# Kernel optimization log

Measured on AMD Instinct MI355X. Metric: run time of the kernel, lower is better.

The kernel has to match this reference:

```python
import jax, jax.numpy as jnp
import numpy as np

B, HW, ENC = 64, 14, 2048
L, V, E, D, A = 20, 10000, 512, 512, 512
T = L - 1  # max decode length (one caption forced to length L)


def setup_inputs() -> dict:
    key = jax.random.key(0)
    ks = jax.random.split(key, 16)

    def p(k, shape, s=0.02):
        return jax.random.normal(k, shape, jnp.float32) * s

    cl = jax.random.randint(ks[2], (B,), 5, L + 1).at[0].set(L)
    return {
        "encoder_out": jax.random.normal(ks[0], (B, HW, HW, ENC), jnp.float32),
        "encoded_captions": jax.random.randint(ks[1], (B, L), 0, V),
        "caption_lengths": cl[:, None].astype(jnp.int32),
        "emb": jax.random.uniform(ks[3], (V, E), jnp.float32, -0.1, 0.1),
        "W_ih": p(ks[4], (4 * D, E + ENC)), "b_ih": jnp.zeros((4 * D,), jnp.float32),
        "W_hh": p(ks[5], (4 * D, D)), "b_hh": jnp.zeros((4 * D,), jnp.float32),
        "W_init_h": p(ks[6], (D, ENC)), "b_init_h": jnp.zeros((D,), jnp.float32),
        "W_init_c": p(ks[7], (D, ENC)), "b_init_c": jnp.zeros((D,), jnp.float32),
        "W_fbeta": p(ks[8], (ENC, D)), "b_fbeta": jnp.zeros((ENC,), jnp.float32),
        "W_fc": jax.random.uniform(ks[9], (V, D), jnp.float32, -0.1, 0.1), "b_fc": jnp.zeros((V,), jnp.float32),
        "W_enc_att": p(ks[10], (A, ENC)), "b_enc_att": jnp.zeros((A,), jnp.float32),
        "W_dec_att": p(ks[11], (A, D)), "b_dec_att": jnp.zeros((A,), jnp.float32),
        "W_full_att": p(ks[12], (1, A)), "b_full_att": jnp.zeros((1,), jnp.float32),
    }


def _decode(encoder_out, encoded_captions, caption_lengths, emb,
            W_ih, b_ih, W_hh, b_hh, W_init_h, b_init_h, W_init_c, b_init_c,
            W_fbeta, b_fbeta, W_fc, b_fc, W_enc_att, b_enc_att,
            W_dec_att, b_dec_att, W_full_att, b_full_att):
    b = encoder_out.shape[0]
    enc = encoder_out.reshape(b, -1, encoder_out.shape[-1])  # [B, P, ENC]
    cl = caption_lengths[:, 0]
    sort_ind = jnp.argsort(-cl)  # descending by caption length
    cl = cl[sort_ind]
    enc = enc[sort_ind]
    caps = encoded_captions[sort_ind]
    decode_lengths = cl - 1  # per-sample number of decode steps

    mean_enc = jnp.mean(enc, axis=1)  # [B, ENC]
    h0 = mean_enc @ W_init_h.T + b_init_h
    c0 = mean_enc @ W_init_c.T + b_init_c

    embeddings = emb[caps]  # [B, L, E]
    # encoder-side attention projection is h-independent: precompute once
    att1 = jnp.einsum('bpe,ae->bpa', enc, W_enc_att) + b_enc_att  # [B, P, A]

    xs_emb = jnp.swapaxes(embeddings[:, :T], 0, 1)  # [T, B, E]
    masks = decode_lengths[None, :] > jnp.arange(T)[:, None]  # [T, B]
    # Note: torch slices h[:batch_size_t]; since batch is length-sorted descending,
    # masking inactive rows (freeze state, zero outputs) computes identical values.

    def step(carry, xs):
        h, c = carry
        emb_t, mask = xs
        # Bahdanau soft attention
        att2 = h @ W_dec_att.T + b_dec_att  # [B, A]
        e = jnp.einsum('bpa,a->bp', jnp.tanh(att1 + att2[:, None, :]), W_full_att[0]) + b_full_att[0]
        alpha = jax.nn.softmax(e, axis=1)  # [B, P]
        awe = jnp.einsum('bp,bpe->be', alpha, enc)  # [B, ENC]
        gate = jax.nn.sigmoid(h @ W_fbeta.T + b_fbeta)
        x = jnp.concatenate([emb_t, gate * awe], axis=1)  # [B, E+ENC]
        # LSTMCell (torch gate order: i, f, g, o)
        gates = x @ W_ih.T + b_ih + h @ W_hh.T + b_hh
        i, f, g, o = jnp.split(gates, 4, axis=1)
        c_new = jax.nn.sigmoid(f) * c + jax.nn.sigmoid(i) * jnp.tanh(g)
        h_new = jax.nn.sigmoid(o) * jnp.tanh(c_new)
        preds = h_new @ W_fc.T + b_fc  # dropout = identity in eval
        m = mask[:, None]
        h = jnp.where(m, h_new, h)
        c = jnp.where(m, c_new, c)
        return (h, c), (jnp.where(m, preds, 0.0), jnp.where(m, alpha, 0.0))

    (_, _), (preds, alphas) = jax.lax.scan(step, (h0, c0), (xs_emb, masks))
    predictions = jnp.swapaxes(preds, 0, 1)  # [B, T, V]
    alphas = jnp.swapaxes(alphas, 0, 1)      # [B, T, P]
    return predictions, caps, alphas, sort_ind


def reference(encoder_out, encoded_captions, caption_lengths, emb,
              W_ih, b_ih, W_hh, b_hh, W_init_h, b_init_h, W_init_c, b_init_c,
              W_fbeta, b_fbeta, W_fc, b_fc, W_enc_att, b_enc_att,
              W_dec_att, b_dec_att, W_full_att, b_full_att):
    return _decode(encoder_out, encoded_captions, caption_lengths, emb,
                   W_ih, b_ih, W_hh, b_hh, W_init_h, b_init_h, W_init_c, b_init_c,
                   W_fbeta, b_fbeta, W_fc, b_fc, W_enc_att, b_enc_att,
                   W_dec_att, b_dec_att, W_full_att, b_full_att)
```

## Files before the change

kernel.cpp:

```cpp
#include <hip/hip_runtime.h>
#include <math.h>

#define Bb 64
#define Pp 196
#define ENCd 2048
#define Lc 20
#define Tt 19
#define Vv 10000
#define Ee 512
#define Dd 512
#define Aa 512
#define K2 2560
#define KG 3072
#define G4 2048

#define OUT_PRED 0ll
#define OUT_CAPS 12160000ll
#define OUT_ALPH 12161280ll
#define OUT_SIND 12399616ll

typedef unsigned short ushort_t;
typedef __attribute__((ext_vector_type(8))) short short8;
typedef __attribute__((ext_vector_type(4))) float f32x4;

#define MFMA16 __builtin_amdgcn_mfma_f32_16x16x32_bf16

__device__ __forceinline__ float b2f(ushort_t u) {
    union { unsigned int i; float f; } x; x.i = ((unsigned int)u) << 16; return x.f;
}
__device__ __forceinline__ ushort_t f2b(float f) {
    union { float f; unsigned int i; } x; x.f = f;
    unsigned int r = x.i + 0x7fffu + ((x.i >> 16) & 1u);
    return (ushort_t)(r >> 16);
}
__device__ __forceinline__ float fsig(float x) { return 1.0f / (1.0f + __expf(-x)); }
__device__ __forceinline__ float ftanh(float x) {
    x = fminf(fmaxf(x, -15.0f), 15.0f);
    float e = __expf(2.0f * x);
    return (e - 1.0f) / (e + 1.0f);
}

__global__ void k_sort(const int* __restrict__ cap_len, const int* __restrict__ caps_in,
                       float* __restrict__ out, int* __restrict__ sind,
                       int* __restrict__ dlen, int* __restrict__ caps_s) {
    __shared__ int cls[Bb];
    int i = threadIdx.x;
    int cl = cap_len[i];
    cls[i] = cl;
    __syncthreads();
    int rank = 0;
    for (int j = 0; j < Bb; ++j) {
        int cj = cls[j];
        rank += (cj > cl) || (cj == cl && j < i);
    }
    sind[rank] = i;
    dlen[rank] = cl - 1;
    out[OUT_SIND + rank] = (float)i;
    for (int l = 0; l < Lc; ++l) {
        int v = caps_in[i * Lc + l];
        caps_s[rank * Lc + l] = v;
        out[OUT_CAPS + rank * Lc + l] = (float)v;
    }
}

__device__ __forceinline__ void cvtseg(const float* __restrict__ src, ushort_t* __restrict__ dst,
                                       int cols, int stride, int off, int bid0, long long quads) {
    long long qid = (long long)bid0 * 256 + threadIdx.x;
    if (qid >= quads) return;
    int c4pr = cols >> 2;
    int r = (int)(qid / c4pr), c4 = (int)(qid % c4pr) << 2;
    float4 v = *(const float4*)&src[(size_t)r * cols + c4];
    ushort4 o; o.x = f2b(v.x); o.y = f2b(v.y); o.z = f2b(v.z); o.w = f2b(v.w);
    *(ushort4*)&dst[(size_t)r * stride + off + c4] = o;
}

__global__ void k_cvtall(const float* Wdec, const float* Wfb, const float* Wih,
                         const float* Whh, const float* Wfc, const float* Wenc_f,
                         const float* Wih0, const float* Wic0,
                         ushort_t* W_ag, ushort_t* W_cat, ushort_t* W_fcb,
                         ushort_t* W_enc, ushort_t* W_hcb) {
    int b = blockIdx.x;
    if      (b < 256)   cvtseg(Wdec,  W_ag,               512,  512,  0,    b,         65536);
    else if (b < 1280)  cvtseg(Wfb,   W_ag + 512 * 512,   512,  512,  0,    b - 256,   262144);
    else if (b < 6400)  cvtseg(Wih,   W_cat,              2560, 3072, 0,    b - 1280,  1310720);
    else if (b < 7424)  cvtseg(Whh,   W_cat,              512,  3072, 2560, b - 6400,  262144);
    else if (b < 12424) cvtseg(Wfc,   W_fcb,              512,  512,  0,    b - 7424,  1280000);
    else if (b < 13448) cvtseg(Wenc_f,W_enc,              2048, 2048, 0,    b - 12424, 262144);
    else if (b < 14472) cvtseg(Wih0,  W_hcb,              2048, 2048, 0,    b - 13448, 262144);
    else                cvtseg(Wic0,  W_hcb + 512 * 2048, 2048, 2048, 0,    b - 14472, 262144);
}

__global__ void k_bias(const float* b_dec, const float* b_fb, const float* b_ihp,
                       const float* b_hhp, const float* b_h, const float* b_c,
                       float* b_ag, float* bsum, float* b_hc) {
    int id = blockIdx.x * 256 + threadIdx.x;
    if (id < 512) b_ag[id] = b_dec[id];
    else if (id < 2560) b_ag[id] = b_fb[id - 512];
    if (id < 2048) bsum[id] = b_ihp[id] + b_hhp[id];
    if (id < 512) b_hc[id] = b_h[id];
    else if (id < 1024) b_hc[id] = b_c[id - 512];
}

__global__ void __launch_bounds__(256) k_enccvt(const float* __restrict__ enc,
                                                const int* __restrict__ sind,
                                                ushort_t* __restrict__ enc_bf) {
    int r = blockIdx.x;
    int b = r / Pp;
    size_t srow = (size_t)sind[b] * Pp + (r - b * Pp);
    int e8 = threadIdx.x * 8;
    const float* s = enc + srow * ENCd + e8;
    float4 v0 = *(const float4*)s;
    float4 v1 = *(const float4*)(s + 4);
    short8 o;
    o[0] = (short)f2b(v0.x); o[1] = (short)f2b(v0.y); o[2] = (short)f2b(v0.z); o[3] = (short)f2b(v0.w);
    o[4] = (short)f2b(v1.x); o[5] = (short)f2b(v1.y); o[6] = (short)f2b(v1.z); o[7] = (short)f2b(v1.w);
    *(short8*)&enc_bf[(size_t)r * ENCd + e8] = o;
}

__global__ void __launch_bounds__(1024) k_meanenc(const ushort_t* __restrict__ enc_bf,
                                                  ushort_t* __restrict__ mean_bf) {
    int b = blockIdx.x;
    int lane = threadIdx.x & 63, w = threadIdx.x >> 6;
    int cg = w & 3, pg = w >> 2;
    int lc = cg * 512 + lane * 8;
    __shared__ float red[4][2048];
    float acc[8] = {};
    for (int p = pg; p < Pp; p += 4) {
        short8 v = *(const short8*)&enc_bf[((size_t)b * Pp + p) * ENCd + lc];
        #pragma unroll
        for (int j = 0; j < 8; ++j) acc[j] += b2f((ushort_t)v[j]);
    }
    #pragma unroll
    for (int j = 0; j < 8; ++j) red[pg][lc + j] = acc[j];
    __syncthreads();
    int tid = threadIdx.x;
    float2 s = {0.f, 0.f};
    #pragma unroll
    for (int g = 0; g < 4; ++g) {
        float2 v = *(const float2*)&red[g][tid * 2];
        s.x += v.x; s.y += v.y;
    }
    ushort2 o; o.x = f2b(s.x * (1.0f / Pp)); o.y = f2b(s.y * (1.0f / Pp));
    *(ushort2*)&mean_bf[(size_t)b * ENCd + tid * 2] = o;
}

__global__ void __launch_bounds__(256) k_att1(const ushort_t* __restrict__ enc_bf,
                                              const ushort_t* __restrict__ Wenc,
                                              const float* __restrict__ benc,
                                              ushort_t* __restrict__ att1) {
    __shared__ ushort_t As[128 * 64];
    __shared__ ushort_t Bs[128 * 64];
    int tid = threadIdx.x;
    int lane = tid & 63, w = tid >> 6;
    int wr = w >> 1, wc = w & 1;
    int m0 = blockIdx.y * 128, n0 = blockIdx.x * 128;
    int r16 = lane & 15;
    f32x4 acc[4][4];
    #pragma unroll
    for (int mf = 0; mf < 4; ++mf)
        #pragma unroll
        for (int nf = 0; nf < 4; ++nf) acc[mf][nf] = (f32x4){0.f, 0.f, 0.f, 0.f};

    int lrow = lane >> 3;
    int lslot = lane & 7;
    for (int k0 = 0; k0 < ENCd; k0 += 64) {
        __syncthreads();
        #pragma unroll
        for (int c = 0; c < 4; ++c) {
            int row = c * 32 + w * 8 + lrow;
            int kg = lslot ^ (row & 7);
            const ushort_t* asrc = enc_bf + (size_t)(m0 + row) * ENCd + k0 + kg * 8;
            const ushort_t* bsrc = Wenc   + (size_t)(n0 + row) * ENCd + k0 + kg * 8;
            __builtin_amdgcn_global_load_lds(
                (const __attribute__((address_space(1))) void*)asrc,
                (__attribute__((address_space(3))) void*)&As[(c * 32 + w * 8) * 64], 16, 0, 0);
            __builtin_amdgcn_global_load_lds(
                (const __attribute__((address_space(1))) void*)bsrc,
                (__attribute__((address_space(3))) void*)&Bs[(c * 32 + w * 8) * 64], 16, 0, 0);
        }
        __syncthreads();
        #pragma unroll
        for (int ks = 0; ks < 2; ++ks) {
            int sl = ks * 4 + (lane >> 4);
            short8 a[4], b[4];
            #pragma unroll
            for (int mf = 0; mf < 4; ++mf) {
                int row = wr * 64 + mf * 16 + r16;
                a[mf] = *(const short8*)&As[row * 64 + ((sl ^ (row & 7)) << 3)];
            }
            #pragma unroll
            for (int nf = 0; nf < 4; ++nf) {
                int row = wc * 64 + nf * 16 + r16;
                b[nf] = *(const short8*)&Bs[row * 64 + ((sl ^ (row & 7)) << 3)];
            }
            #pragma unroll
            for (int mf = 0; mf < 4; ++mf)
                #pragma unroll
                for (int nf = 0; nf < 4; ++nf)
                    acc[mf][nf] = MFMA16(a[mf], b[nf], acc[mf][nf], 0, 0, 0);
        }
    }
    int rj0 = (lane >> 4) << 2;
    #pragma unroll
    for (int mf = 0; mf < 4; ++mf)
        #pragma unroll
        for (int nf = 0; nf < 4; ++nf) {
            int col = n0 + wc * 64 + nf * 16 + r16;
            float bv = benc[col];
            #pragma unroll
            for (int j = 0; j < 4; ++j) {
                int row = m0 + wr * 64 + mf * 16 + rj0 + j;
                att1[(size_t)row * Aa + col] = f2b(acc[mf][nf][j] + bv);
            }
        }
}

__global__ void __launch_bounds__(256) k_h0c0(
        const ushort_t* __restrict__ A, const ushort_t* __restrict__ W,
        const float* __restrict__ bias, ushort_t* __restrict__ hout,
        float* __restrict__ cst) {
    int lane = threadIdx.x & 63, w = threadIdx.x >> 6;
    int r16 = lane & 15, kq = (lane >> 4) << 3;
    int ncol[4];
    #pragma unroll
    for (int tt = 0; tt < 4; ++tt) ncol[tt] = blockIdx.x * 64 + tt * 16 + r16;
    f32x4 acc[4][4];
    #pragma unroll
    for (int mt = 0; mt < 4; ++mt)
        #pragma unroll
        for (int tt = 0; tt < 4; ++tt) acc[mt][tt] = (f32x4){0.f, 0.f, 0.f, 0.f};
    for (int k0 = w * 512; k0 < w * 512 + 512; k0 += 32) {
        short8 a[4];
        #pragma unroll
        for (int mt = 0; mt < 4; ++mt)
            a[mt] = *(const short8*)(A + (size_t)(mt * 16 + r16) * ENCd + k0 + kq);
        #pragma unroll
        for (int tt = 0; tt < 4; ++tt) {
            short8 bw = *(const short8*)&W[(size_t)ncol[tt] * ENCd + k0 + kq];
            #pragma unroll
            for (int mt = 0; mt < 4; ++mt)
                acc[mt][tt] = MFMA16(a[mt], bw, acc[mt][tt], 0, 0, 0);
        }
    }
    __shared__ float red[2][64][68];
    if (w >= 2) {
        float* row = &red[w - 2][lane][0];
        #pragma unroll
        for (int mt = 0; mt < 4; ++mt)
            #pragma unroll
            for (int tt = 0; tt < 4; ++tt) *(f32x4*)&row[(mt * 4 + tt) * 4] = acc[mt][tt];
    }
    __syncthreads();
    if (w < 2) {
        float* row = &red[w][lane][0];
        #pragma unroll
        for (int mt = 0; mt < 4; ++mt)
            #pragma unroll
            for (int tt = 0; tt < 4; ++tt) acc[mt][tt] += *(f32x4*)&row[(mt * 4 + tt) * 4];
    }
    __syncthreads();
    if (w == 1) {
        float* row = &red[0][lane][0];
        #pragma unroll
        for (int mt = 0; mt < 4; ++mt)
            #pragma unroll
            for (int tt = 0; tt < 4; ++tt) *(f32x4*)&row[(mt * 4 + tt) * 4] = acc[mt][tt];
    }
    __syncthreads();
    if (w != 0) return;
    {
        float* row = &red[0][lane][0];
        #pragma unroll
        for (int mt = 0; mt < 4; ++mt)
            #pragma unroll
            for (int tt = 0; tt < 4; ++tt) acc[mt][tt] += *(f32x4*)&row[(mt * 4 + tt) * 4];
    }
    int rj0 = (lane >> 4) << 2;
    #pragma unroll
    for (int mt = 0; mt < 4; ++mt)
        #pragma unroll
        for (int tt = 0; tt < 4; ++tt) {
            int col = ncol[tt];
            float bv = bias[col];
            #pragma unroll
            for (int j = 0; j < 4; ++j) {
                int row = mt * 16 + rj0 + j;
                float v = acc[mt][tt][j] + bv;
                if (col < 512) hout[row * Dd + col] = f2b(v);
                else           cst[row * Dd + (col - 512)] = v;
            }
        }
}

__global__ void __launch_bounds__(256) k_ag(
        const ushort_t* __restrict__ h, const ushort_t* __restrict__ W,
        const float* __restrict__ bias, float* __restrict__ of) {
    int lane = threadIdx.x & 63, w = threadIdx.x >> 6;
    int r16 = lane & 15, kq = (lane >> 4) << 3;
    int col = blockIdx.x * 16 + r16;
    f32x4 acc[4];
    #pragma unroll
    for (int mt = 0; mt < 4; ++mt) acc[mt] = (f32x4){0.f, 0.f, 0.f, 0.f};
    for (int k0 = w * 128; k0 < w * 128 + 128; k0 += 32) {
        short8 bw = *(const short8*)&W[(size_t)col * Dd + k0 + kq];
        #pragma unroll
        for (int mt = 0; mt < 4; ++mt) {
            short8 a = *(const short8*)(h + (size_t)(mt * 16 + r16) * Dd + k0 + kq);
            acc[mt] = MFMA16(a, bw, acc[mt], 0, 0, 0);
        }
    }
    __shared__ float red[2][64][20];
    if (w >= 2) {
        float* rr = &red[w - 2][lane][0];
        #pragma unroll
        for (int mt = 0; mt < 4; ++mt) *(f32x4*)&rr[mt * 4] = acc[mt];
    }
    __syncthreads();
    if (w < 2) {
        float* rr = &red[w][lane][0];
        #pragma unroll
        for (int mt = 0; mt < 4; ++mt) acc[mt] += *(f32x4*)&rr[mt * 4];
    }
    __syncthreads();
    if (w == 1) {
        float* rr = &red[0][lane][0];
        #pragma unroll
        for (int mt = 0; mt < 4; ++mt) *(f32x4*)&rr[mt * 4] = acc[mt];
    }
    __syncthreads();
    if (w != 0) return;
    {
        float* rr = &red[0][lane][0];
        #pragma unroll
        for (int mt = 0; mt < 4; ++mt) acc[mt] += *(f32x4*)&rr[mt * 4];
    }
    int rj0 = (lane >> 4) << 2;
    float bv = bias[col];
    #pragma unroll
    for (int mt = 0; mt < 4; ++mt)
        #pragma unroll
        for (int j = 0; j < 4; ++j) {
            int row = mt * 16 + rj0 + j;
            float v = acc[mt][j] + bv;
            of[(size_t)row * K2 + col] = (col >= 512) ? fsig(v) : v;
        }
}

__global__ void __launch_bounds__(1024) k_esmawe(
        const ushort_t* __restrict__ att1, const float* __restrict__ ag,
        const float* __restrict__ wfull, const float* __restrict__ bfull,
        const ushort_t* __restrict__ enc_bf,
        const float* __restrict__ emb, const int* __restrict__ caps_s,
        ushort_t* __restrict__ x2, float* __restrict__ out,
        const int* __restrict__ dlen, int t) {
    int b = blockIdx.x;
    int tid = threadIdx.x;
    int lane = tid & 63, wv = tid >> 6;
    __shared__ float att2f[512], wfl[512];
    __shared__ float e_sh[200], al_sh[200], sm[4];
    __shared__ float redA[4][2048];
    if (tid < 512) att2f[tid] = ag[(size_t)b * K2 + tid];
    else           wfl[tid - 512] = wfull[tid - 512];
    __syncthreads();
    float a2[8], wf8[8];
    #pragma unroll
    for (int j = 0; j < 8; ++j) { a2[j] = att2f[lane * 8 + j]; wf8[j] = wfl[lane * 8 + j]; }
    float bf0 = bfull[0];
    for (int p0 = wv; p0 < Pp; p0 += 32) {
        int p1 = p0 + 16;
        bool has1 = p1 < Pp;
        short8 v0 = *(const short8*)&att1[((size_t)b * Pp + p0) * Aa + lane * 8];
        short8 v1 = has1 ? *(const short8*)&att1[((size_t)b * Pp + p1) * Aa + lane * 8] : v0;
        float s0 = 0.f, s1 = 0.f;
        #pragma unroll
        for (int j = 0; j < 8; ++j) {
            s0 += ftanh(b2f((ushort_t)v0[j]) + a2[j]) * wf8[j];
            s1 += ftanh(b2f((ushort_t)v1[j]) + a2[j]) * wf8[j];
        }
        #pragma unroll
        for (int o = 32; o; o >>= 1) {
            s0 += __shfl_xor(s0, o);
            s1 += __shfl_xor(s1, o);
        }
        if (lane == 0) {
            e_sh[p0] = s0 + bf0;
            if (has1) e_sh[p1] = s1 + bf0;
        }
    }
    __syncthreads();
    if (wv == 0) {
        float v0 = e_sh[lane];
        float v1 = e_sh[lane + 64];
        float v2 = e_sh[lane + 128];
        float v3 = (lane + 192 < Pp) ? e_sh[lane + 192] : -1e30f;
        float m = fmaxf(fmaxf(v0, v1), fmaxf(v2, v3));
        #pragma unroll
        for (int o = 32; o; o >>= 1) m = fmaxf(m, __shfl_xor(m, o));
        float ss = __expf(v0 - m) + __expf(v1 - m) + __expf(v2 - m) + __expf(v3 - m);
        #pragma unroll
        for (int o = 32; o; o >>= 1) ss += __shfl_xor(ss, o);
        if (lane == 0) { sm[0] = m; sm[1] = 1.0f / ss; }
    } else if (tid >= 512 && tid < 768) {
        int q = tid - 512;
        float2 e2v = *(const float2*)&emb[(size_t)caps_s[b * Lc + t] * Ee + q * 2];
        ushort2 o2; o2.x = f2b(e2v.x); o2.y = f2b(e2v.y);
        *(ushort2*)&x2[(size_t)b * K2 + q * 2] = o2;
    }
    __syncthreads();
    float mx = sm[0], inv = sm[1];
    if (tid < Pp) {
        float al = __expf(e_sh[tid] - mx) * inv;
        al_sh[tid] = al;
        out[OUT_ALPH + ((long long)b * Tt + t) * Pp + tid] = (t < dlen[b]) ? al : 0.0f;
    }
    __syncthreads();
    {
        int cg = tid & 255, pg = tid >> 8;
        int c0 = cg * 8;
        float acc[8] = {};
        const ushort_t* ep = enc_bf + (size_t)b * Pp * ENCd + c0;
        for (int p = pg; p < Pp; p += 4) {
            float a = al_sh[p];
            short8 vv = *(const short8*)(ep + (size_t)p * ENCd);
            #pragma unroll
            for (int j = 0; j < 8; ++j) acc[j] += a * b2f((ushort_t)vv[j]);
        }
        *(f32x4*)&redA[pg][c0]     = *(f32x4*)&acc[0];
        *(f32x4*)&redA[pg][c0 + 4] = *(f32x4*)&acc[4];
    }
    __syncthreads();
    {
        int c2 = tid * 2;
        float s0 = redA[0][c2] + redA[1][c2] + redA[2][c2] + redA[3][c2];
        float s1 = redA[0][c2 + 1] + redA[1][c2 + 1] + redA[2][c2 + 1] + redA[3][c2 + 1];
        float2 g2 = *(const float2*)&ag[(size_t)b * K2 + 512 + c2];
        ushort2 o2; o2.x = f2b(g2.x * s0); o2.y = f2b(g2.y * s1);
        *(ushort2*)&x2[(size_t)b * K2 + Ee + c2] = o2;
    }
}

__global__ void __launch_bounds__(512) k_gates(
        const ushort_t* __restrict__ x2, const ushort_t* __restrict__ hin,
        const ushort_t* __restrict__ Wcat, const float* __restrict__ bsum,
        ushort_t* __restrict__ hout, float* __restrict__ cst,
        const int* __restrict__ dlen, int t) {
    int lane = threadIdx.x & 63, w = threadIdx.x >> 6;
    int r16 = lane & 15, kq = (lane >> 4) << 3;
    int m0 = blockIdx.y * 16;
    int d0 = blockIdx.x * 16;
    int row = m0 + r16;
    f32x4 acc[4];
    #pragma unroll
    for (int tt = 0; tt < 4; ++tt) acc[tt] = (f32x4){0.f, 0.f, 0.f, 0.f};
    for (int k0 = w * 384; k0 < w * 384 + 384; k0 += 32) {
        const ushort_t* s = (k0 < K2) ? (x2 + (size_t)row * K2 + k0 + kq)
                                      : (hin + (size_t)row * Dd + (k0 - K2) + kq);
        short8 a = *(const short8*)s;
        #pragma unroll
        for (int tt = 0; tt < 4; ++tt) {
            short8 bw = *(const short8*)&Wcat[(size_t)(d0 + tt * 512 + r16) * KG + k0 + kq];
            acc[tt] = MFMA16(a, bw, acc[tt], 0, 0, 0);
        }
    }
    __shared__ float red[4][64][20];
    for (int s2 = 4; s2; s2 >>= 1) {
        if (w >= s2 && w < 2 * s2) {
            float* rr = &red[w - s2][lane][0];
            #pragma unroll
            for (int tt = 0; tt < 4; ++tt) *(f32x4*)&rr[tt * 4] = acc[tt];
        }
        __syncthreads();
        if (w < s2) {
            float* rr = &red[w][lane][0];
            #pragma unroll
            for (int tt = 0; tt < 4; ++tt) acc[tt] += *(f32x4*)&rr[tt * 4];
        }
        __syncthreads();
    }
    if (w != 0) return;
    int rj0 = (lane >> 4) << 2;
    int d = d0 + r16;
    #pragma unroll
    for (int j = 0; j < 4; ++j) {
        int rw = m0 + rj0 + j;
        ushort_t hb;
        if (t < dlen[rw]) {
            float gi = acc[0][j] + bsum[d];
            float gf = acc[1][j] + bsum[512 + d];
            float gg = acc[2][j] + bsum[1024 + d];
            float go = acc[3][j] + bsum[1536 + d];
            float cv = cst[rw * Dd + d];
            float cn = fsig(gf) * cv + fsig(gi) * ftanh(gg);
            cst[rw * Dd + d] = cn;
            hb = f2b(fsig(go) * ftanh(cn));
        } else {
            hb = hin[rw * Dd + d];
        }
        hout[rw * Dd + d] = hb;
    }
}

__global__ void __launch_bounds__(256) k_preds(
        const ushort_t* __restrict__ hball, const ushort_t* __restrict__ Wfc,
        const float* __restrict__ bfc, const int* __restrict__ dlen,
        float* __restrict__ out) {
    int lane = threadIdx.x & 63, w = threadIdx.x >> 6;
    int r16 = lane & 15, kq = (lane >> 4) << 3, rj0 = (lane >> 4) << 2;
    int ts = blockIdx.y * 4 + w;
    if (ts >= Tt) return;
    int n0 = blockIdx.x * 80;
    f32x4 acc[4][5];
    #pragma unroll
    for (int mt = 0; mt < 4; ++mt)
        #pragma unroll
        for (int tt = 0; tt < 5; ++tt) acc[mt][tt] = (f32x4){0.f, 0.f, 0.f, 0.f};
    const ushort_t* ap = hball + (size_t)((ts + 1) * Bb + r16) * Dd + kq;
    for (int k0 = 0; k0 < Dd; k0 += 32) {
        short8 a[4];
        #pragma unroll
        for (int mt = 0; mt < 4; ++mt)
            a[mt] = *(const short8*)(ap + (size_t)(mt * 16) * Dd + k0);
        #pragma unroll
        for (int tt = 0; tt < 5; ++tt) {
            short8 bw = *(const short8*)&Wfc[(size_t)(n0 + tt * 16 + r16) * Dd + k0 + kq];
            #pragma unroll
            for (int mt = 0; mt < 4; ++mt)
                acc[mt][tt] = MFMA16(a[mt], bw, acc[mt][tt], 0, 0, 0);
        }
    }
    #pragma unroll
    for (int tt = 0; tt < 5; ++tt) {
        int col = n0 + tt * 16 + r16;
        float bv = bfc[col];
        #pragma unroll
        for (int mt = 0; mt < 4; ++mt)
            #pragma unroll
            for (int j = 0; j < 4; ++j) {
                int b = mt * 16 + rj0 + j;
                out[OUT_PRED + ((long long)b * Tt + ts) * Vv + col] =
                    (ts < dlen[b]) ? acc[mt][tt][j] + bv : 0.0f;
            }
    }
}

extern "C" void kernel_launch(void* const* d_in, const int* in_sizes, int n_in,
                              void* d_out, int out_size, void* d_ws, size_t ws_size,
                              hipStream_t stream) {
    const float* encoder_out      = (const float*)d_in[0];
    const int*   encoded_captions = (const int*)d_in[1];
    const int*   caption_lengths  = (const int*)d_in[2];
    const float* emb       = (const float*)d_in[3];
    const float* W_ih      = (const float*)d_in[4];
    const float* b_ih      = (const float*)d_in[5];
    const float* W_hh      = (const float*)d_in[6];
    const float* b_hh      = (const float*)d_in[7];
    const float* W_init_h  = (const float*)d_in[8];
    const float* b_init_h  = (const float*)d_in[9];
    const float* W_init_c  = (const float*)d_in[10];
    const float* b_init_c  = (const float*)d_in[11];
    const float* W_fbeta   = (const float*)d_in[12];
    const float* b_fbeta   = (const float*)d_in[13];
    const float* W_fc      = (const float*)d_in[14];
    const float* b_fc      = (const float*)d_in[15];
    const float* W_enc_att = (const float*)d_in[16];
    const float* b_enc_att = (const float*)d_in[17];
    const float* W_dec_att = (const float*)d_in[18];
    const float* b_dec_att = (const float*)d_in[19];
    const float* W_full_att = (const float*)d_in[20];
    const float* b_full_att = (const float*)d_in[21];
    float* out = (float*)d_out;

    char* p = (char*)d_ws;
    auto alloc = [&](size_t bytes) { char* r = p; p += (bytes + 255) & ~255ull; return r; };
    int* sind   = (int*)alloc(64 * 4);
    int* dlen   = (int*)alloc(64 * 4);
    int* caps_s = (int*)alloc(Bb * Lc * 4);
    float* c_st  = (float*)alloc(Bb * Dd * 4);
    float* ag    = (float*)alloc((size_t)Bb * K2 * 4);
    float* b_ag  = (float*)alloc(K2 * 4);
    float* bsum  = (float*)alloc(G4 * 4);
    float* b_hc  = (float*)alloc(1024 * 4);
    ushort_t* mean_bf = (ushort_t*)alloc((size_t)Bb * ENCd * 2);
    ushort_t* hball   = (ushort_t*)alloc((size_t)(Tt + 1) * Bb * Dd * 2);
    ushort_t* x2      = (ushort_t*)alloc((size_t)Bb * K2 * 2);
    ushort_t* att1    = (ushort_t*)alloc((size_t)Bb * Pp * Aa * 2);
    ushort_t* W_enc   = (ushort_t*)alloc((size_t)Aa * ENCd * 2);
    ushort_t* W_ag    = (ushort_t*)alloc((size_t)K2 * Dd * 2);
    ushort_t* W_cat   = (ushort_t*)alloc((size_t)G4 * KG * 2);
    ushort_t* W_fcb   = (ushort_t*)alloc((size_t)Vv * Dd * 2);
    ushort_t* W_hcb   = (ushort_t*)alloc((size_t)1024 * ENCd * 2);
    ushort_t* enc_bf  = (ushort_t*)alloc((size_t)Bb * Pp * ENCd * 2);

    k_sort<<<1, 64, 0, stream>>>(caption_lengths, encoded_captions, out, sind, dlen, caps_s);
    k_cvtall<<<15496, 256, 0, stream>>>(W_dec_att, W_fbeta, W_ih, W_hh, W_fc, W_enc_att,
                                        W_init_h, W_init_c, W_ag, W_cat, W_fcb, W_enc, W_hcb);
    k_bias<<<10, 256, 0, stream>>>(b_dec_att, b_fbeta, b_ih, b_hh, b_init_h, b_init_c,
                                   b_ag, bsum, b_hc);
    k_enccvt<<<12544, 256, 0, stream>>>(encoder_out, sind, enc_bf);
    k_meanenc<<<64, 1024, 0, stream>>>(enc_bf, mean_bf);
    k_h0c0<<<16, 256, 0, stream>>>(mean_bf, W_hcb, b_hc, hball, c_st);
    k_att1<<<dim3(4, 98), 256, 0, stream>>>(enc_bf, W_enc, b_enc_att, att1);

    for (int t = 0; t < Tt; ++t) {
        const ushort_t* hcur = hball + (size_t)t * Bb * Dd;
        ushort_t* hnext = hball + (size_t)(t + 1) * Bb * Dd;
        k_ag<<<160, 256, 0, stream>>>(hcur, W_ag, b_ag, ag);
        k_esmawe<<<64, 1024, 0, stream>>>(att1, ag, W_full_att, b_full_att, enc_bf,
            emb, caps_s, x2, out, dlen, t);
        k_gates<<<dim3(32, 4), 512, 0, stream>>>(x2, hcur, W_cat, bsum, hnext, c_st, dlen, t);
    }
    k_preds<<<dim3(125, 5), 256, 0, stream>>>(hball, W_fcb, b_fc, dlen, out);
}
```

Before: 1.388 ms.

## Split attention-weighted encoding across four blocks per sample; stage pred stores via LDS

The attention kernel now launches four blocks per batch row. Each block recomputes the scores and softmax, then reduces only a 512-channel slice of the encoder, which raises parallelism from 64 to 256 blocks but repeats the score computation four times. Separately, the prediction kernel stages each MFMA tile in shared memory so it can write coalesced 16-byte nontemporal stores instead of scattered scalar stores. The LDS handoff in the prediction kernel relies on lgkmcnt waits within a single wave rather than a barrier.

```diff
diff --git a/kernel.cpp b/kernel.cpp
--- a/kernel.cpp
+++ b/kernel.cpp
@@ -353,12 +353,12 @@
         const float* __restrict__ emb, const int* __restrict__ caps_s,
         ushort_t* __restrict__ x2, float* __restrict__ out,
         const int* __restrict__ dlen, int t) {
-    int b = blockIdx.x;
+    int b = blockIdx.x >> 2, ch = blockIdx.x & 3;
     int tid = threadIdx.x;
     int lane = tid & 63, wv = tid >> 6;
     __shared__ float att2f[512], wfl[512];
     __shared__ float e_sh[200], al_sh[200], sm[4];
-    __shared__ float redA[4][2048];
+    __shared__ float redA[16][512];
     if (tid < 512) att2f[tid] = ag[(size_t)b * K2 + tid];
     else           wfl[tid - 512] = wfull[tid - 512];
     __syncthreads();
@@ -400,7 +400,7 @@
         #pragma unroll
         for (int o = 32; o; o >>= 1) ss += __shfl_xor(ss, o);
         if (lane == 0) { sm[0] = m; sm[1] = 1.0f / ss; }
-    } else if (tid >= 512 && tid < 768) {
+    } else if (ch == 0 && tid >= 512 && tid < 768) {
         int q = tid - 512;
         float2 e2v = *(const float2*)&emb[(size_t)caps_s[b * Lc + t] * Ee + q * 2];
         ushort2 o2; o2.x = f2b(e2v.x); o2.y = f2b(e2v.y);
@@ -411,15 +411,16 @@
     if (tid < Pp) {
         float al = __expf(e_sh[tid] - mx) * inv;
         al_sh[tid] = al;
-        out[OUT_ALPH + ((long long)b * Tt + t) * Pp + tid] = (t < dlen[b]) ? al : 0.0f;
+        if (ch == 0)
+            out[OUT_ALPH + ((long long)b * Tt + t) * Pp + tid] = (t < dlen[b]) ? al : 0.0f;
     }
     __syncthreads();
     {
-        int cg = tid & 255, pg = tid >> 8;
+        int cg = tid & 63, pg = tid >> 6;
         int c0 = cg * 8;
         float acc[8] = {};
-        const ushort_t* ep = enc_bf + (size_t)b * Pp * ENCd + c0;
-        for (int p = pg; p < Pp; p += 4) {
+        const ushort_t* ep = enc_bf + (size_t)b * Pp * ENCd + ch * 512 + c0;
+        for (int p = pg; p < Pp; p += 16) {
             float a = al_sh[p];
             short8 vv = *(const short8*)(ep + (size_t)p * ENCd);
             #pragma unroll
@@ -429,13 +430,13 @@
         *(f32x4*)&redA[pg][c0 + 4] = *(f32x4*)&acc[4];
     }
     __syncthreads();
-    {
-        int c2 = tid * 2;
-        float s0 = redA[0][c2] + redA[1][c2] + redA[2][c2] + redA[3][c2];
-        float s1 = redA[0][c2 + 1] + redA[1][c2 + 1] + redA[2][c2 + 1] + redA[3][c2 + 1];
-        float2 g2 = *(const float2*)&ag[(size_t)b * K2 + 512 + c2];
-        ushort2 o2; o2.x = f2b(g2.x * s0); o2.y = f2b(g2.y * s1);
-        *(ushort2*)&x2[(size_t)b * K2 + Ee + c2] = o2;
+    if (tid < 512) {
+        float s = 0.f;
+        #pragma unroll
+        for (int g = 0; g < 16; ++g) s += redA[g][tid];
+        int col = ch * 512 + tid;
+        float gte = ag[(size_t)b * K2 + 512 + col];
+        x2[(size_t)b * K2 + Ee + col] = f2b(gte * s);
     }
 }
 
@@ -504,6 +505,7 @@
         const ushort_t* __restrict__ hball, const ushort_t* __restrict__ Wfc,
         const float* __restrict__ bfc, const int* __restrict__ dlen,
         float* __restrict__ out) {
+    __shared__ float lds[4][16][84];
     int lane = threadIdx.x & 63, w = threadIdx.x >> 6;
     int r16 = lane & 15, kq = (lane >> 4) << 3, rj0 = (lane >> 4) << 2;
     int ts = blockIdx.y * 4 + w;
@@ -529,17 +531,26 @@
         }
     }
     #pragma unroll
-    for (int tt = 0; tt < 5; ++tt) {
-        int col = n0 + tt * 16 + r16;
-        float bv = bfc[col];
-        #pragma unroll
-        for (int mt = 0; mt < 4; ++mt)
-            #pragma unroll
-            for (int j = 0; j < 4; ++j) {
-                int b = mt * 16 + rj0 + j;
-                out[OUT_PRED + ((long long)b * Tt + ts) * Vv + col] =
-                    (ts < dlen[b]) ? acc[mt][tt][j] + bv : 0.0f;
-            }
+    for (int mt = 0; mt < 4; ++mt) {
+        #pragma unroll
+        for (int tt = 0; tt < 5; ++tt) {
+            float bv = bfc[n0 + tt * 16 + r16];
+            #pragma unroll
+            for (int j = 0; j < 4; ++j)
+                lds[w][rj0 + j][tt * 16 + r16] = acc[mt][tt][j] + bv;
+        }
+        asm volatile("s_waitcnt lgkmcnt(0)" ::: "memory");
+        #pragma unroll
+        for (int c = 0; c < 5; ++c) {
+            int idx = c * 64 + lane;
+            int row = idx / 20, c4 = idx % 20;
+            int b = mt * 16 + row;
+            f32x4 v = *(f32x4*)&lds[w][row][c4 * 4];
+            if (ts >= dlen[b]) v = (f32x4){0.f, 0.f, 0.f, 0.f};
+            __builtin_nontemporal_store(v,
+                (f32x4*)&out[OUT_PRED + ((long long)b * Tt + ts) * Vv + n0 + c4 * 4]);
+        }
+        asm volatile("s_waitcnt vmcnt(0)" ::: "memory");
     }
 }
 
@@ -605,7 +616,7 @@
         const ushort_t* hcur = hball + (size_t)t * Bb * Dd;
         ushort_t* hnext = hball + (size_t)(t + 1) * Bb * Dd;
         k_ag<<<160, 256, 0, stream>>>(hcur, W_ag, b_ag, ag);
-        k_esmawe<<<64, 1024, 0, stream>>>(att1, ag, W_full_att, b_full_att, enc_bf,
+        k_esmawe<<<256, 1024, 0, stream>>>(att1, ag, W_full_att, b_full_att, enc_bf,
             emb, caps_s, x2, out, dlen, t);
         k_gates<<<dim3(32, 4), 512, 0, stream>>>(x2, hcur, W_cat, bsum, hnext, c_st, dlen, t);
     }
```

Result: faster. 1.184 ms (-14.7%).
